# Kernel tuning notes

Hardware: AMD Instinct MI355X
Metric: run time of the kernel (lower is better)

## Reference

```python
import jax, jax.numpy as jnp
import numpy as np

N = 50000      # num nodes
E = 800000     # edges per hypergraph (avg degree 16)
G = 3          # hyper_edge_num
D_IN = 128
D_OUT = 128


def setup_inputs() -> dict:
    key = jax.random.key(0)
    ks = jax.random.split(key, 6)
    company_emb = jax.random.normal(ks[0], (N, D_IN), dtype=jnp.float32)
    # nn.Linear weight [out, in], glorot-ish scaling
    W = jax.random.normal(ks[1], (D_OUT, D_IN), dtype=jnp.float32) / np.sqrt(D_IN).astype(np.float32)
    alpha = jax.random.normal(ks[2], (G, 1), dtype=jnp.float32)
    edge_rows = jax.random.randint(ks[3], (G, E), 0, N, dtype=jnp.int32)
    edge_cols = jax.random.randint(ks[4], (G, E), 0, N, dtype=jnp.int32)
    edge_vals = jax.random.normal(ks[5], (G, E), dtype=jnp.float32)
    return {
        "company_emb": company_emb,
        "W": W,
        "alpha": alpha,
        "edge_rows": edge_rows,
        "edge_cols": edge_cols,
        "edge_vals": edge_vals,
    }


def reference(company_emb, W, alpha, edge_rows, edge_cols, edge_vals):
    # shared dense projection: h = X @ W^T, [N, D_OUT]
    h = company_emb @ W.T

    def spmm(rows, cols, vals):
        # sparse Laplacian (COO) @ h : gather source rows, scale, scatter-add to dest rows
        msg = vals[:, None] * h[cols]                     # [E, D_OUT]
        return jax.ops.segment_sum(msg, rows, num_segments=N)

    aggs = jax.vmap(spmm)(edge_rows, edge_cols, edge_vals)  # [G, N, D_OUT]
    gate = jax.nn.sigmoid(alpha[:, 0])                       # [G]
    # res = sum_g sigmoid(alpha_g) * (L_g @ h)
    return jnp.einsum('g,gnd->nd', gate, aggs)
```

## Files before the change

### kernel.cpp

```cpp
#include <hip/hip_runtime.h>
#include <math.h>

#define NNODES 50000
#define NEDGE  800000
#define NG     3
#define GE     (NG*NEDGE)
#define NBUK   1536
#define OS     (NBUK + 1)
#define CH     4688
#define NBLK   512
#define GBLK   391
#define FGRID  (GBLK + NBLK)
#define STGCAP 1920
#define NPH    7
#define MAXG   231
#define SCAP   2624

typedef __attribute__((ext_vector_type(8))) short bf16x8;
typedef __attribute__((ext_vector_type(4))) float f32x4;

__device__ __forceinline__ unsigned short f2bf(float f) {
    unsigned u = __float_as_uint(f);
    return (unsigned short)((u + 0x7fffu + ((u >> 16) & 1u)) >> 16);
}

__device__ __forceinline__ int bucket_of(unsigned r) {
    return (int)((r * 96u) / 3125u);
}

__global__ __launch_bounds__(512) void k_front(const float* __restrict__ X,
                                               const float* __restrict__ W,
                                               const int* __restrict__ rows,
                                               const int* __restrict__ cols,
                                               const float* __restrict__ vals,
                                               const float* __restrict__ alpha,
                                               unsigned short* __restrict__ hb16,
                                               uint2* __restrict__ out1,
                                               unsigned short* __restrict__ off1) {
    __shared__ __align__(16) char smem[53024];
    const int t = threadIdx.x;

    if (blockIdx.x < GBLK) {
        uint4* Wl = (uint4*)smem;
        for (int i = t; i < 2048; i += 512) {
            const int nt   = i >> 8;
            const int kc   = (i >> 6) & 3;
            const int lane = i & 63;
            const int n  = nt * 16 + (lane & 15);
            const int k0 = kc * 32 + (lane >> 4) * 8;
            const float* src = W + (size_t)n * 128 + k0;
            float4 a = *(const float4*)(src);
            float4 b = *(const float4*)(src + 4);
            unsigned u0 = (unsigned)f2bf(a.x) | ((unsigned)f2bf(a.y) << 16);
            unsigned u1 = (unsigned)f2bf(a.z) | ((unsigned)f2bf(a.w) << 16);
            unsigned u2 = (unsigned)f2bf(b.x) | ((unsigned)f2bf(b.y) << 16);
            unsigned u3 = (unsigned)f2bf(b.z) | ((unsigned)f2bf(b.w) << 16);
            Wl[i] = make_uint4(u0, u1, u2, u3);
        }
        __syncthreads();

        const int w    = t >> 6;
        const int lane = t & 63;
        const int q    = lane >> 4;
        const int ml   = lane & 15;
        const int m0   = blockIdx.x * 128 + w * 16;

        int xr = m0 + ml; if (xr >= NNODES) xr = NNODES - 1;
        const float* xrow = X + (size_t)xr * 128;

        bf16x8 xf[4];
#pragma unroll
        for (int kc = 0; kc < 4; ++kc) {
            const int k0 = kc * 32 + q * 8;
            float4 a = *(const float4*)(xrow + k0);
            float4 b = *(const float4*)(xrow + k0 + 4);
            bf16x8 v;
            v[0] = (short)f2bf(a.x); v[1] = (short)f2bf(a.y);
            v[2] = (short)f2bf(a.z); v[3] = (short)f2bf(a.w);
            v[4] = (short)f2bf(b.x); v[5] = (short)f2bf(b.y);
            v[6] = (short)f2bf(b.z); v[7] = (short)f2bf(b.w);
            xf[kc] = v;
        }

        f32x4 acc[8];
#pragma unroll
        for (int nt = 0; nt < 8; ++nt) acc[nt] = (f32x4){0.f, 0.f, 0.f, 0.f};
#pragma unroll
        for (int nt = 0; nt < 8; ++nt)
#pragma unroll
            for (int kc = 0; kc < 4; ++kc) {
                const bf16x8 wf = *(const bf16x8*)&Wl[(nt * 4 + kc) * 64 + lane];
                acc[nt] = __builtin_amdgcn_mfma_f32_16x16x32_bf16(xf[kc], wf, acc[nt], 0, 0, 0);
            }
        __syncthreads();

        unsigned short* hst = (unsigned short*)smem + w * 2176;
#pragma unroll
        for (int nt = 0; nt < 8; ++nt)
#pragma unroll
            for (int r = 0; r < 4; ++r)
                hst[(q * 4 + r) * 136 + nt * 16 + ml] = f2bf(acc[nt][r]);
        __syncthreads();

#pragma unroll
        for (int i = 0; i < 4; ++i) {
            const int chunk = i * 64 + lane;
            const int lr    = chunk >> 4;
            const int cc    = chunk & 15;
            const int row   = m0 + lr;
            const uint4 v = *(const uint4*)(hst + lr * 136 + cc * 8);
            if (row < NNODES)
                ((uint4*)(hb16 + (size_t)row * 128))[cc] = v;
        }
    } else {
        uint2*          stg = (uint2*)smem;
        unsigned short* rnk = (unsigned short*)(smem + 37504);
        int*            sA  = (int*)(smem + 46880);
        const int bb    = blockIdx.x - GBLK;
        const int start = bb * CH;
        const int end   = (start + CH < GE) ? (start + CH) : GE;
        const int len   = end - start;

        const float g0 = 1.0f / (1.0f + __expf(-alpha[0]));
        const float g1 = 1.0f / (1.0f + __expf(-alpha[1]));
        const float g2 = 1.0f / (1.0f + __expf(-alpha[2]));

#pragma unroll
        for (int j = 0; j < 3; ++j) sA[t + j * 512] = 0;
        __syncthreads();

        for (int k = t; k < len; k += 512) {
            const int idx = start + k;
            const int r = rows[idx];
            const int c = cols[idx];
            const float v = vals[idx];
            const float gv = v * (idx < NEDGE ? g0 : (idx < 2 * NEDGE ? g1 : g2));
            uint2 rec;
            rec.x = ((unsigned)r << 16) | (unsigned)c;
            rec.y = __float_as_uint(gv);
            stg[k] = rec;
            rnk[k] = (unsigned short)atomicAdd(&sA[bucket_of((unsigned)r)], 1);
        }
        __syncthreads();

        for (int off = 1; off < 1536; off <<= 1) {
            int v[3];
#pragma unroll
            for (int j = 0; j < 3; ++j) {
                const int i = t + j * 512;
                v[j] = sA[i] + ((i >= off) ? sA[i - off] : 0);
            }
            __syncthreads();
#pragma unroll
            for (int j = 0; j < 3; ++j) sA[t + j * 512] = v[j];
            __syncthreads();
        }

        if (t < NBUK) off1[(size_t)bb * OS + t] = (unsigned short)(t ? sA[t - 1] : 0);
        for (int b = t + 512; b < NBUK; b += 512)
            off1[(size_t)bb * OS + b] = (unsigned short)sA[b - 1];
        if (t == 0) off1[(size_t)bb * OS + NBUK] = (unsigned short)sA[NBUK - 1];

        for (int k = t; k < len; k += 512) {
            const uint2 rec = stg[k];
            const int b = bucket_of(rec.x >> 16);
            const int pos = (b ? sA[b - 1] : 0) + (int)rnk[k];
            out1[(size_t)bb * CH + pos] = rec;
        }
    }
}

__global__ __launch_bounds__(512, 8) void k_agg(const unsigned* __restrict__ hbits,
                                                const uint2* __restrict__ out1,
                                                const unsigned short* __restrict__ off1,
                                                float* __restrict__ out) {
    __shared__ __align__(16) uint2          stg[STGCAP];
    __shared__ __align__(16) unsigned short colS[SCAP];
    __shared__ __align__(16) float          valS[SCAP];
    __shared__ int rh[MAXG], grpBase[MAXG + 1], gcur[MAXG];
    __shared__ int sA[512];
    const int t = threadIdx.x;
    const int b = blockIdx.x;

    const int sstart = (b * 3125 + 95) / 96;
    const int send   = ((b + 1) * 3125 + 95) / 96;
    const int width  = send - sstart;
    const int ngrp   = NPH * width;

    if (t < MAXG) rh[t] = 0;

    const int s0 = off1[(size_t)t * OS + b];
    const int e0 = off1[(size_t)t * OS + b + 1];
    const int len = e0 - s0;
    sA[t] = len;
    __syncthreads();

    for (int off = 1; off < 512; off <<= 1) {
        const int v = sA[t] + ((t >= off) ? sA[t - off] : 0);
        __syncthreads();
        sA[t] = v;
        __syncthreads();
    }
    const int base = sA[t] - len;
    __syncthreads();

    {
        const uint2* seg = out1 + (size_t)t * CH;
        int p = base;
        for (int i = s0; i < e0; ++i, ++p) {
            const uint2 rec = seg[i];
            if (p < STGCAP) {
                stg[p] = rec;
                const int lr = (int)(rec.x >> 16) - sstart;
                const int ph = (int)((rec.x & 0xffffu) >> 13);
                atomicAdd(&rh[ph * width + lr], 1);
            }
        }
    }
    __syncthreads();

    if (t < 256) sA[t] = (t < ngrp) ? ((rh[t] + 3) & ~3) : 0;
    __syncthreads();
    for (int off = 1; off < 256; off <<= 1) {
        int v = 0;
        if (t < 256) v = sA[t] + ((t >= off) ? sA[t - off] : 0);
        __syncthreads();
        if (t < 256) sA[t] = v;
        __syncthreads();
    }
    if (t < ngrp) {
        const int pc = (rh[t] + 3) & ~3;
        const int gb = sA[t] - pc;
        grpBase[t] = gb;
        gcur[t]    = gb;
        for (int k = gb + rh[t]; k < gb + pc; ++k) { colS[k] = 0; valS[k] = 0.f; }
    }
    if (t == 0) grpBase[MAXG] = 0;
    if (t == 256 - 1) {  }
    __syncthreads();
    if (t == 0) grpBase[ngrp] = sA[ngrp - 1];
    __syncthreads();

    {
        const int lim = (base + len < STGCAP) ? (base + len) : STGCAP;
        for (int k = base; k < lim; ++k) {
            const uint2 rec = stg[k];
            const int lr = (int)(rec.x >> 16) - sstart;
            const int ph = (int)((rec.x & 0xffffu) >> 13);
            const int pos = atomicAdd(&gcur[ph * width + lr], 1);
            colS[pos] = (unsigned short)(rec.x & 0xffffu);
            valS[pos] = __uint_as_float(rec.y);
        }
    }
    __syncthreads();

    const int w    = t >> 6;
    const int lane = t & 63;
    float2 acc[5];
#pragma unroll
    for (int ri = 0; ri < 5; ++ri) acc[ri] = make_float2(0.f, 0.f);

    for (int ph = 0; ph < NPH; ++ph) {
#pragma unroll
        for (int ri = 0; ri < 5; ++ri) {
            const int lr = w + ri * 8;
            if (lr < width) {
                const int g = ph * width + lr;
                const int s = grpBase[g];
                const int e = grpBase[g + 1];
                int i = s;
                for (; i + 8 <= e; i += 8) {
                    const uint2  ca = *(const uint2*)&colS[i];
                    const uint2  cb = *(const uint2*)&colS[i + 4];
                    const float4 v0 = *(const float4*)&valS[i];
                    const float4 v1 = *(const float4*)&valS[i + 4];
                    unsigned hb[8];
                    hb[0] = hbits[(size_t)(ca.x & 0xffffu) * 64 + lane];
                    hb[1] = hbits[(size_t)(ca.x >> 16)     * 64 + lane];
                    hb[2] = hbits[(size_t)(ca.y & 0xffffu) * 64 + lane];
                    hb[3] = hbits[(size_t)(ca.y >> 16)     * 64 + lane];
                    hb[4] = hbits[(size_t)(cb.x & 0xffffu) * 64 + lane];
                    hb[5] = hbits[(size_t)(cb.x >> 16)     * 64 + lane];
                    hb[6] = hbits[(size_t)(cb.y & 0xffffu) * 64 + lane];
                    hb[7] = hbits[(size_t)(cb.y >> 16)     * 64 + lane];
                    const float vv[8] = {v0.x, v0.y, v0.z, v0.w, v1.x, v1.y, v1.z, v1.w};
#pragma unroll
                    for (int j = 0; j < 8; ++j) {
                        acc[ri].x += vv[j] * __uint_as_float(hb[j] << 16);
                        acc[ri].y += vv[j] * __uint_as_float(hb[j] & 0xffff0000u);
                    }
                }
                if (i < e) {
                    const uint2  ca = *(const uint2*)&colS[i];
                    const float4 v0 = *(const float4*)&valS[i];
                    unsigned hb[4];
                    hb[0] = hbits[(size_t)(ca.x & 0xffffu) * 64 + lane];
                    hb[1] = hbits[(size_t)(ca.x >> 16)     * 64 + lane];
                    hb[2] = hbits[(size_t)(ca.y & 0xffffu) * 64 + lane];
                    hb[3] = hbits[(size_t)(ca.y >> 16)     * 64 + lane];
                    const float vv[4] = {v0.x, v0.y, v0.z, v0.w};
#pragma unroll
                    for (int j = 0; j < 4; ++j) {
                        acc[ri].x += vv[j] * __uint_as_float(hb[j] << 16);
                        acc[ri].y += vv[j] * __uint_as_float(hb[j] & 0xffff0000u);
                    }
                }
            }
        }
    }

#pragma unroll
    for (int ri = 0; ri < 5; ++ri) {
        const int lr = w + ri * 8;
        if (lr < width) {
            const int row = sstart + lr;
            ((float2*)out)[(size_t)row * 64 + lane] = acc[ri];
        }
    }
}

extern "C" void kernel_launch(void* const* d_in, const int* in_sizes, int n_in,
                              void* d_out, int out_size, void* d_ws, size_t ws_size,
                              hipStream_t stream) {
    const float* X     = (const float*)d_in[0];
    const float* W     = (const float*)d_in[1];
    const float* alpha = (const float*)d_in[2];
    const int*   rows  = (const int*)d_in[3];
    const int*   cols  = (const int*)d_in[4];
    const float* vals  = (const float*)d_in[5];
    float* out = (float*)d_out;

    char* ws = (char*)d_ws;
    unsigned*       hbits = (unsigned*)(ws + 0);
    unsigned short* hb16  = (unsigned short*)(ws + 0);
    uint2*          out1  = (uint2*)(ws + 12800000);
    unsigned short* off1  = (unsigned short*)(ws + 32002048);

    hipLaunchKernelGGL(k_front, dim3(FGRID), dim3(512), 0, stream,
                       X, W, rows, cols, vals, alpha, hb16, out1, off1);
    hipLaunchKernelGGL(k_agg, dim3(NBUK), dim3(512), 0, stream,
                       hbits, out1, off1, out);
}
```

Baseline: 212.8 us.

## Rebalance bucketing to 2048 buckets and drop LDS record staging in sort

The edge-partition stage now uses 400 chunks of 6000 edges and 2048 destination buckets, so each aggregation block handles about 24 rows instead of about 33. The partition pass no longer stages full records in LDS. It first counts bucket ranks from rows alone, then re-reads rows, cols and vals from global memory to scatter the records. This cuts LDS use in the front kernel and should raise occupancy, at the cost of reading rows twice. With more, smaller aggregation blocks, each block also has less staging work and smaller LDS buffers.

```diff
diff --git a/kernel.cpp b/kernel.cpp
--- a/kernel.cpp
+++ b/kernel.cpp
@@ -5,16 +5,16 @@
 #define NEDGE  800000
 #define NG     3
 #define GE     (NG*NEDGE)
-#define NBUK   1536
+#define NBUK   2048
 #define OS     (NBUK + 1)
-#define CH     4688
-#define NBLK   512
+#define CH     6000
+#define NBLK   400
 #define GBLK   391
 #define FGRID  (GBLK + NBLK)
-#define STGCAP 1920
+#define STGCAP 1536
 #define NPH    7
-#define MAXG   231
-#define SCAP   2624
+#define MAXG   175
+#define SCAP   2112
 
 typedef __attribute__((ext_vector_type(8))) short bf16x8;
 typedef __attribute__((ext_vector_type(4))) float f32x4;
@@ -25,7 +25,7 @@
 }
 
 __device__ __forceinline__ int bucket_of(unsigned r) {
-    return (int)((r * 96u) / 3125u);
+    return (int)((r * 128u) / 3125u);
 }
 
 __global__ __launch_bounds__(512) void k_front(const float* __restrict__ X,
@@ -37,7 +37,7 @@
                                                unsigned short* __restrict__ hb16,
                                                uint2* __restrict__ out1,
                                                unsigned short* __restrict__ off1) {
-    __shared__ __align__(16) char smem[53024];
+    __shared__ __align__(16) char smem[34816];
     const int t = threadIdx.x;
 
     if (blockIdx.x < GBLK) {
@@ -113,58 +113,53 @@
                 ((uint4*)(hb16 + (size_t)row * 128))[cc] = v;
         }
     } else {
-        uint2*          stg = (uint2*)smem;
-        unsigned short* rnk = (unsigned short*)(smem + 37504);
-        int*            sA  = (int*)(smem + 46880);
+        unsigned short* rnk = (unsigned short*)smem;
+        int*            sA  = (int*)(smem + 12032);
         const int bb    = blockIdx.x - GBLK;
         const int start = bb * CH;
-        const int end   = (start + CH < GE) ? (start + CH) : GE;
-        const int len   = end - start;
 
         const float g0 = 1.0f / (1.0f + __expf(-alpha[0]));
         const float g1 = 1.0f / (1.0f + __expf(-alpha[1]));
         const float g2 = 1.0f / (1.0f + __expf(-alpha[2]));
 
 #pragma unroll
-        for (int j = 0; j < 3; ++j) sA[t + j * 512] = 0;
-        __syncthreads();
-
-        for (int k = t; k < len; k += 512) {
+        for (int j = 0; j < 4; ++j) sA[t + j * 512] = 0;
+        __syncthreads();
+
+        for (int k = t; k < CH; k += 512) {
+            const int r = rows[start + k];
+            rnk[k] = (unsigned short)atomicAdd(&sA[bucket_of((unsigned)r)], 1);
+        }
+        __syncthreads();
+
+        for (int off = 1; off < 2048; off <<= 1) {
+            int v[4];
+#pragma unroll
+            for (int j = 0; j < 4; ++j) {
+                const int i = t + j * 512;
+                v[j] = sA[i] + ((i >= off) ? sA[i - off] : 0);
+            }
+            __syncthreads();
+#pragma unroll
+            for (int j = 0; j < 4; ++j) sA[t + j * 512] = v[j];
+            __syncthreads();
+        }
+
+        for (int b = t; b < NBUK; b += 512)
+            off1[(size_t)bb * OS + b] = (unsigned short)(b ? sA[b - 1] : 0);
+        if (t == 0) off1[(size_t)bb * OS + NBUK] = (unsigned short)sA[NBUK - 1];
+
+        for (int k = t; k < CH; k += 512) {
             const int idx = start + k;
             const int r = rows[idx];
             const int c = cols[idx];
             const float v = vals[idx];
             const float gv = v * (idx < NEDGE ? g0 : (idx < 2 * NEDGE ? g1 : g2));
+            const int b = bucket_of((unsigned)r);
+            const int pos = (b ? sA[b - 1] : 0) + (int)rnk[k];
             uint2 rec;
             rec.x = ((unsigned)r << 16) | (unsigned)c;
             rec.y = __float_as_uint(gv);
-            stg[k] = rec;
-            rnk[k] = (unsigned short)atomicAdd(&sA[bucket_of((unsigned)r)], 1);
-        }
-        __syncthreads();
-
-        for (int off = 1; off < 1536; off <<= 1) {
-            int v[3];
-#pragma unroll
-            for (int j = 0; j < 3; ++j) {
-                const int i = t + j * 512;
-                v[j] = sA[i] + ((i >= off) ? sA[i - off] : 0);
-            }
-            __syncthreads();
-#pragma unroll
-            for (int j = 0; j < 3; ++j) sA[t + j * 512] = v[j];
-            __syncthreads();
-        }
-
-        if (t < NBUK) off1[(size_t)bb * OS + t] = (unsigned short)(t ? sA[t - 1] : 0);
-        for (int b = t + 512; b < NBUK; b += 512)
-            off1[(size_t)bb * OS + b] = (unsigned short)sA[b - 1];
-        if (t == 0) off1[(size_t)bb * OS + NBUK] = (unsigned short)sA[NBUK - 1];
-
-        for (int k = t; k < len; k += 512) {
-            const uint2 rec = stg[k];
-            const int b = bucket_of(rec.x >> 16);
-            const int pos = (b ? sA[b - 1] : 0) + (int)rnk[k];
             out1[(size_t)bb * CH + pos] = rec;
         }
     }
@@ -182,15 +177,18 @@
     const int t = threadIdx.x;
     const int b = blockIdx.x;
 
-    const int sstart = (b * 3125 + 95) / 96;
-    const int send   = ((b + 1) * 3125 + 95) / 96;
+    const int sstart = (b * 3125 + 127) >> 7;
+    const int send   = ((b + 1) * 3125 + 127) >> 7;
     const int width  = send - sstart;
     const int ngrp   = NPH * width;
 
     if (t < MAXG) rh[t] = 0;
 
-    const int s0 = off1[(size_t)t * OS + b];
-    const int e0 = off1[(size_t)t * OS + b + 1];
+    int s0 = 0, e0 = 0;
+    if (t < NBLK) {
+        s0 = off1[(size_t)t * OS + b];
+        e0 = off1[(size_t)t * OS + b + 1];
+    }
     const int len = e0 - s0;
     sA[t] = len;
     __syncthreads();
@@ -235,8 +233,6 @@
         gcur[t]    = gb;
         for (int k = gb + rh[t]; k < gb + pc; ++k) { colS[k] = 0; valS[k] = 0.f; }
     }
-    if (t == 0) grpBase[MAXG] = 0;
-    if (t == 256 - 1) {  }
     __syncthreads();
     if (t == 0) grpBase[ngrp] = sA[ngrp - 1];
     __syncthreads();
@@ -256,13 +252,13 @@
 
     const int w    = t >> 6;
     const int lane = t & 63;
-    float2 acc[5];
-#pragma unroll
-    for (int ri = 0; ri < 5; ++ri) acc[ri] = make_float2(0.f, 0.f);
+    float2 acc[4];
+#pragma unroll
+    for (int ri = 0; ri < 4; ++ri) acc[ri] = make_float2(0.f, 0.f);
 
     for (int ph = 0; ph < NPH; ++ph) {
 #pragma unroll
-        for (int ri = 0; ri < 5; ++ri) {
+        for (int ri = 0; ri < 4; ++ri) {
             const int lr = w + ri * 8;
             if (lr < width) {
                 const int g = ph * width + lr;
@@ -310,7 +306,7 @@
     }
 
 #pragma unroll
-    for (int ri = 0; ri < 5; ++ri) {
+    for (int ri = 0; ri < 4; ++ri) {
         const int lr = w + ri * 8;
         if (lr < width) {
             const int row = sstart + lr;
@@ -334,7 +330,7 @@
     unsigned*       hbits = (unsigned*)(ws + 0);
     unsigned short* hb16  = (unsigned short*)(ws + 0);
     uint2*          out1  = (uint2*)(ws + 12800000);
-    unsigned short* off1  = (unsigned short*)(ws + 32002048);
+    unsigned short* off1  = (unsigned short*)(ws + 32000000);
 
     hipLaunchKernelGGL(k_front, dim3(FGRID), dim3(512), 0, stream,
                        X, W, rows, cols, vals, alpha, hb16, out1, off1);
```

After: 212.5 us. Within noise of the previous version (-0.1%).
